# Kernel optimization log

Hardware: AMD Instinct MI355X
Metric: run time of the kernel (lower is better)

Reference implementation:

```python
import jax, jax.numpy as jnp
import numpy as np

N, E = 50000, 800000
IN_F, C, H, OUT_F = 128, 32, 4, 4
HC = H * C
EPS = 1e-5


def gatv2(x, src, dst, ea, Wl, Wr, We, att, bias, concat):
    # x: [N, in], ea: [E, 1], Wl/Wr: [in, H*C], We: [1, H*C], att: [h, C]
    h, c = att.shape
    xl = (x @ Wl).reshape(-1, h, c)          # [N, h, c]
    xr = (x @ Wr).reshape(-1, h, c)          # [N, h, c]
    m = xl[src] + xr[dst] + (ea @ We).reshape(-1, h, c)   # [E, h, c]
    e = jnp.einsum('ehc,hc->eh', jax.nn.leaky_relu(m, 0.2), att)  # [E, h]
    emax = jax.ops.segment_max(e, dst, num_segments=N)
    e = jnp.exp(e - emax[dst])
    denom = jax.ops.segment_sum(e, dst, num_segments=N)
    alpha = e / (denom[dst] + 1e-16)         # [E, h]
    out = jax.ops.segment_sum(alpha[:, :, None] * xl[src], dst, num_segments=N)  # [N, h, c]
    out = out.reshape(N, h * c) if concat else out.mean(axis=1)
    return out + bias


def bn_eval(x, g, b, m, v):
    return (x - m) * jax.lax.rsqrt(v + EPS) * g + b


def setup_inputs() -> dict:
    key = jax.random.key(0)
    ks = iter(jax.random.split(key, 40))
    nrm = lambda shape, s=0.2: jax.random.normal(next(ks), shape, jnp.float32) * s
    d = {}
    d['x'] = jax.random.normal(next(ks), (N, IN_F), jnp.float32)
    d['edge_index'] = jax.random.randint(next(ks), (2, E), 0, N, jnp.int32)
    d['edge_attr'] = jax.random.normal(next(ks), (E, 1), jnp.float32)
    # layer 1
    d['l1_Wl'] = nrm((IN_F, HC)); d['l1_Wr'] = nrm((IN_F, HC))
    d['l1_We'] = nrm((1, HC)); d['l1_att'] = nrm((H, C)); d['l1_b'] = nrm((HC,))
    # layers 2-9 stacked
    d['mid_Wl'] = nrm((8, HC, HC)); d['mid_Wr'] = nrm((8, HC, HC))
    d['mid_We'] = nrm((8, 1, HC)); d['mid_att'] = nrm((8, H, C)); d['mid_b'] = nrm((8, HC))
    # layer 10: heads=1, concat=False
    d['l10_Wl'] = nrm((HC, C)); d['l10_Wr'] = nrm((HC, C))
    d['l10_We'] = nrm((1, C)); d['l10_att'] = nrm((1, C)); d['l10_b'] = nrm((C,))
    # batchnorms (eval mode): bn1-9 stacked, bn10 separate
    d['bn_g'] = jax.random.uniform(next(ks), (9, HC), jnp.float32, 0.5, 1.5)
    d['bn_b'] = nrm((9, HC)); d['bn_m'] = nrm((9, HC))
    d['bn_v'] = jax.random.uniform(next(ks), (9, HC), jnp.float32, 0.5, 1.5)
    d['bn10_g'] = jax.random.uniform(next(ks), (C,), jnp.float32, 0.5, 1.5)
    d['bn10_b'] = nrm((C,)); d['bn10_m'] = nrm((C,))
    d['bn10_v'] = jax.random.uniform(next(ks), (C,), jnp.float32, 0.5, 1.5)
    d['lin_W'] = nrm((C, OUT_F)); d['lin_b'] = nrm((OUT_F,))
    return d


def reference(x, edge_index, edge_attr,
              l1_Wl, l1_Wr, l1_We, l1_att, l1_b,
              mid_Wl, mid_Wr, mid_We, mid_att, mid_b,
              l10_Wl, l10_Wr, l10_We, l10_att, l10_b,
              bn_g, bn_b, bn_m, bn_v,
              bn10_g, bn10_b, bn10_m, bn10_v,
              lin_W, lin_b):
    src, dst = edge_index[0], edge_index[1]
    h = jax.nn.relu(gatv2(x, src, dst, edge_attr, l1_Wl, l1_Wr, l1_We, l1_att, l1_b, True))
    h = bn_eval(h, bn_g[0], bn_b[0], bn_m[0], bn_v[0])
    for i in range(8):  # layers 2-9
        h = jax.nn.relu(gatv2(h, src, dst, edge_attr, mid_Wl[i], mid_Wr[i], mid_We[i], mid_att[i], mid_b[i], True))
        h = bn_eval(h, bn_g[i + 1], bn_b[i + 1], bn_m[i + 1], bn_v[i + 1])
    h = jax.nn.relu(gatv2(h, src, dst, edge_attr, l10_Wl, l10_Wr, l10_We, l10_att, l10_b, False))
    h = bn_eval(h, bn10_g, bn10_b, bn10_m, bn10_v)
    return h @ lin_W + lin_b
```

## Files before the change

### kernel.cpp

```cpp
#include <hip/hip_runtime.h>
#include <math.h>

#define NN 50000
#define EE 800000
#define EPS 1e-5f
#define SCAN_CH 196

#define NEG_BIG (-1e30f)
#define RESCALE_THR 4.0f

#define LO_SCALE 2048.0f
#define LO_INV   (1.0f/2048.0f)

typedef unsigned short u16;
typedef _Float16 f16x8 __attribute__((ext_vector_type(8)));
typedef float f32x4 __attribute__((ext_vector_type(4)));

__device__ __forceinline__ u16 f2h(float f) {
    _Float16 h = (_Float16)f;
    return __builtin_bit_cast(u16, h);
}
__device__ __forceinline__ float h2f(u16 u) {
    return (float)__builtin_bit_cast(_Float16, u);
}

__global__ void hist_kernel(const int* __restrict__ dst, int* cnt) {
    int e = blockIdx.x * blockDim.x + threadIdx.x;
    if (e < EE) atomicAdd(&cnt[dst[e]], 1);
}

__global__ void scan_part(const int* __restrict__ cnt, int* __restrict__ part) {
    __shared__ int red[256];
    int b = blockIdx.x, t = threadIdx.x;
    int i = b * SCAN_CH + t;
    int v = (t < SCAN_CH && i < NN) ? cnt[i] : 0;
    red[t] = v;
    __syncthreads();
#pragma unroll
    for (int s = 128; s; s >>= 1) {
        if (t < s) red[t] += red[t + s];
        __syncthreads();
    }
    if (t == 0) part[b] = red[0];
}

__global__ void scan_block(int* part) {
    __shared__ int buf[2][256];
    int t = threadIdx.x;
    int v = part[t];
    int p = 0;
    buf[0][t] = v;
    __syncthreads();
#pragma unroll
    for (int off = 1; off < 256; off <<= 1) {
        buf[p ^ 1][t] = buf[p][t] + ((t >= off) ? buf[p][t - off] : 0);
        __syncthreads();
        p ^= 1;
    }
    part[t] = buf[p][t] - v;
}

__global__ void scan_final(int* __restrict__ cntcur, const int* __restrict__ part,
                           int* __restrict__ row_start) {
    __shared__ int buf[2][256];
    int b = blockIdx.x, t = threadIdx.x;
    int i = b * SCAN_CH + t;
    int v = (t < SCAN_CH && i < NN) ? cntcur[i] : 0;
    int p = 0;
    buf[0][t] = v;
    __syncthreads();
#pragma unroll
    for (int off = 1; off < 256; off <<= 1) {
        buf[p ^ 1][t] = buf[p][t] + ((t >= off) ? buf[p][t - off] : 0);
        __syncthreads();
        p ^= 1;
    }
    if (t < SCAN_CH && i < NN) {
        int pos = part[b] + buf[p][t] - v;
        row_start[i] = pos;
        cntcur[i] = pos;
    }
    if (b == 0 && t == 0) row_start[NN] = EE;
}

__global__ void scatter_kernel(const int* __restrict__ ei, const float* __restrict__ ea,
                               int* cursor, int2* __restrict__ edge_pack) {
    int e = blockIdx.x * blockDim.x + threadIdx.x;
    if (e < EE) {
        int d = ei[EE + e];
        int pos = atomicAdd(&cursor[d], 1);
        edge_pack[pos] = make_int2(ei[e], __float_as_int(ea[e]));
    }
}

__global__ void split_f32(const float* __restrict__ in, u16* __restrict__ hi,
                          u16* __restrict__ lo, int n4) {
    int i = blockIdx.x * blockDim.x + threadIdx.x;
    if (i >= n4) return;
    float4 v = ((const float4*)in)[i];
    ushort4 h, l;
    h.x = f2h(v.x); l.x = f2h((v.x - h2f(h.x)) * LO_SCALE);
    h.y = f2h(v.y); l.y = f2h((v.y - h2f(h.y)) * LO_SCALE);
    h.z = f2h(v.z); l.z = f2h((v.z - h2f(h.z)) * LO_SCALE);
    h.w = f2h(v.w); l.w = f2h((v.w - h2f(h.w)) * LO_SCALE);
    ((ushort4*)hi)[i] = h;
    ((ushort4*)lo)[i] = l;
}

__global__ void conv_w(const float* __restrict__ l1Wl, const float* __restrict__ l1Wr,
                       const float* __restrict__ midWl, const float* __restrict__ midWr,
                       u16* __restrict__ Wh, u16* __restrict__ Wlo) {
    int tid = blockIdx.x * 256 + threadIdx.x;
    if (tid >= 9 * 256 * 128) return;
    int L = tid >> 15;
    int rem = tid & 32767;
    int n = rem >> 7, k = rem & 127;
    const float* WL;
    const float* WR;
    if (L == 0) { WL = l1Wl; WR = l1Wr; }
    else {
        WL = midWl + (size_t)(L - 1) * 16384;
        WR = midWr + (size_t)(L - 1) * 16384;
    }
    float w = (n < 128) ? WL[k * 128 + n] : WR[k * 128 + (n - 128)];
    u16 h = f2h(w);
    Wh[tid] = h;
    Wlo[tid] = f2h((w - h2f(h)) * LO_SCALE);
}

__global__ __launch_bounds__(256) void gemm_mfma(const u16* __restrict__ Ah,
                                                 const u16* __restrict__ Al,
                                                 const u16* __restrict__ Bh,
                                                 const u16* __restrict__ Bl,
                                                 float* __restrict__ C) {
    int w    = threadIdx.x >> 6;
    int lane = threadIdx.x & 63;
    int lr = lane & 15;
    int kg = lane >> 4;
    int rowbase = blockIdx.x * 128;
    int colbase = blockIdx.y * 128 + w * 32;

    f16x8 bh[2][4], bl[2][4];
#pragma unroll
    for (int ct = 0; ct < 2; ++ct) {
        size_t boff = (size_t)(colbase + ct * 16 + lr) * 128 + (size_t)(kg * 8);
#pragma unroll
        for (int ks = 0; ks < 4; ++ks) {
            bh[ct][ks] = *(const f16x8*)(Bh + boff + ks * 32);
            bl[ct][ks] = *(const f16x8*)(Bl + boff + ks * 32);
        }
    }

    auto aoff_of = [&](int rt) {
        int arow = rowbase + rt * 16 + lr;
        if (arow >= NN) arow = NN - 1;
        return (size_t)arow * 128 + (size_t)(kg * 8);
    };
    f16x8 ahc[4], alc[4], ahn[4], aln[4];
    {
        size_t ao = aoff_of(0);
#pragma unroll
        for (int ks = 0; ks < 4; ++ks) {
            ahc[ks] = *(const f16x8*)(Ah + ao + ks * 32);
            alc[ks] = *(const f16x8*)(Al + ao + ks * 32);
        }
    }

#pragma unroll
    for (int rt = 0; rt < 8; ++rt) {
        if (rt < 7) {
            size_t ao = aoff_of(rt + 1);
#pragma unroll
            for (int ks = 0; ks < 4; ++ks) {
                ahn[ks] = *(const f16x8*)(Ah + ao + ks * 32);
                aln[ks] = *(const f16x8*)(Al + ao + ks * 32);
            }
        }

        f32x4 aH[2], aL[2];
#pragma unroll
        for (int ct = 0; ct < 2; ++ct) {
            aH[ct] = (f32x4){0.f, 0.f, 0.f, 0.f};
            aL[ct] = (f32x4){0.f, 0.f, 0.f, 0.f};
        }
#pragma unroll
        for (int ks = 0; ks < 4; ++ks) {
#pragma unroll
            for (int ct = 0; ct < 2; ++ct) {
                aH[ct] = __builtin_amdgcn_mfma_f32_16x16x32_f16(ahc[ks], bh[ct][ks], aH[ct], 0, 0, 0);
                aL[ct] = __builtin_amdgcn_mfma_f32_16x16x32_f16(alc[ks], bh[ct][ks], aL[ct], 0, 0, 0);
                aL[ct] = __builtin_amdgcn_mfma_f32_16x16x32_f16(ahc[ks], bl[ct][ks], aL[ct], 0, 0, 0);
            }
        }

        int crow0 = rowbase + rt * 16 + kg * 4;
#pragma unroll
        for (int ct = 0; ct < 2; ++ct) {
            float* cp = C + (size_t)crow0 * 256 + colbase + ct * 16 + lr;
#pragma unroll
            for (int r = 0; r < 4; ++r) {
                if (crow0 + r < NN)
                    cp[(size_t)r * 256] = fmaf(aL[ct][r], LO_INV, aH[ct][r]);
            }
        }

        if (rt < 7) {
#pragma unroll
            for (int ks = 0; ks < 4; ++ks) { ahc[ks] = ahn[ks]; alc[ks] = aln[ks]; }
        }
    }
}

__global__ __launch_bounds__(256) void gemm_tile(const float* __restrict__ A,
                                                 const float* __restrict__ B,
                                                 float* __restrict__ C,
                                                 int M, int nc, int ldb, int ldc, int coff) {
    __shared__ float As[128][64];
    __shared__ float Bs[128][64];
    int t  = threadIdx.x;
    int bm = blockIdx.x * 64;
    int bn = blockIdx.y * 64;
    {
        int k4 = (t & 31) << 2;
        int r0 = t >> 5;
#pragma unroll
        for (int pass = 0; pass < 8; ++pass) {
            int row = r0 + pass * 8;
            int gm  = bm + row;
            float4 v = make_float4(0.f, 0.f, 0.f, 0.f);
            if (gm < M) v = *(const float4*)(A + (size_t)gm * 128 + k4);
            As[k4 + 0][row] = v.x; As[k4 + 1][row] = v.y;
            As[k4 + 2][row] = v.z; As[k4 + 3][row] = v.w;
        }
    }
    {
        int c4 = (t & 15) << 2;
        int kr = t >> 4;
#pragma unroll
        for (int pass = 0; pass < 8; ++pass) {
            int k  = kr + pass * 16;
            int gc = bn + c4;
            float4 v = make_float4(0.f, 0.f, 0.f, 0.f);
            if (gc < nc) v = *(const float4*)(B + (size_t)k * ldb + gc);
            *(float4*)&Bs[k][c4] = v;
        }
    }
    __syncthreads();

    int tx = t & 15, ty = t >> 4;
    int m0 = ty * 4, c0 = tx * 4;
    float acc[4][4] = {{0.f}};
#pragma unroll 8
    for (int k = 0; k < 128; ++k) {
        float4 av = *(const float4*)&As[k][m0];
        float4 bv = *(const float4*)&Bs[k][c0];
        float a4[4] = {av.x, av.y, av.z, av.w};
        float b4[4] = {bv.x, bv.y, bv.z, bv.w};
#pragma unroll
        for (int i = 0; i < 4; ++i)
#pragma unroll
            for (int j = 0; j < 4; ++j) acc[i][j] = fmaf(a4[i], b4[j], acc[i][j]);
    }
#pragma unroll
    for (int i = 0; i < 4; ++i) {
        int gm = bm + m0 + i;
        int gc = bn + c0;
        if (gm < M && gc < nc) {
            *(float4*)(C + (size_t)gm * ldc + coff + gc) =
                make_float4(acc[i][0], acc[i][1], acc[i][2], acc[i][3]);
        }
    }
}

__device__ __forceinline__ float dpp_add8(float x) {
    int t;
    t = __builtin_amdgcn_update_dpp(0, __float_as_int(x), 0xB1, 0xf, 0xf, true);
    x += __int_as_float(t);
    t = __builtin_amdgcn_update_dpp(0, __float_as_int(x), 0x4E, 0xf, 0xf, true);
    x += __int_as_float(t);
    t = __builtin_amdgcn_update_dpp(0, __float_as_int(x), 0x141, 0xf, 0xf, true);
    x += __int_as_float(t);
    return x;
}

__global__ __launch_bounds__(256) void node_agg_128(const float* __restrict__ xlr,
                                                    const int* __restrict__ row_start,
                                                    const int2* __restrict__ epack,
                                                    const float* __restrict__ We,
                                                    const float* __restrict__ att,
                                                    const float* __restrict__ bias,
                                                    const float* __restrict__ bng,
                                                    const float* __restrict__ bnb,
                                                    const float* __restrict__ bnm,
                                                    const float* __restrict__ bnv,
                                                    u16* __restrict__ ahi,
                                                    u16* __restrict__ alo,
                                                    int wf32,
                                                    float* __restrict__ hout) {
    int wave = (blockIdx.x * blockDim.x + threadIdx.x) >> 6;
    int lane = threadIdx.x & 63;
    if (wave >= NN) return;
    int half = lane >> 5;
    int c0   = (lane & 31) << 2;

    const float L2E = 1.44269504f;
    const float4 xr4 = *(const float4*)(xlr + (size_t)wave * 256 + 128 + c0);
    const float4 we4 = *(const float4*)(We + c0);
    const float4 at4 = *(const float4*)(att + c0);
    float4 a6, a4;
    a6.x = 0.6f * L2E * at4.x; a4.x = 0.4f * L2E * at4.x;
    a6.y = 0.6f * L2E * at4.y; a4.y = 0.4f * L2E * at4.y;
    a6.z = 0.6f * L2E * at4.z; a4.z = 0.4f * L2E * at4.z;
    a6.w = 0.6f * L2E * at4.w; a4.w = 0.4f * L2E * at4.w;

    int beg = row_start[wave], end = row_start[wave + 1];
    int lastE = end - 1;

    float mx0 = NEG_BIG, sm0 = 0.f;
    float mx1 = NEG_BIG, sm1 = 0.f;
    float4 ac0 = make_float4(0.f, 0.f, 0.f, 0.f);
    float4 ac1 = make_float4(0.f, 0.f, 0.f, 0.f);

    auto score = [&](float eav, const float4& xv) -> float {
        float m0 = xv.x + fmaf(eav, we4.x, xr4.x);
        float m1 = xv.y + fmaf(eav, we4.y, xr4.y);
        float m2 = xv.z + fmaf(eav, we4.z, xr4.z);
        float m3 = xv.w + fmaf(eav, we4.w, xr4.w);
        float p = fmaf(a6.x, m0, a4.x * fabsf(m0));
        p = fmaf(a6.y, m1, fmaf(a4.y, fabsf(m1), p));
        p = fmaf(a6.z, m2, fmaf(a4.z, fabsf(m2), p));
        p = fmaf(a6.w, m3, fmaf(a4.w, fabsf(m3), p));
        return dpp_add8(p);
    };

    auto upd = [&](float& mx, float& sm, float4& ac, float p, const float4& xv) {
        float d = p - mx;
        if (__ballot(d > RESCALE_THR)) {
            float nm = fmaxf(mx, p);
            float sc = exp2f(mx - nm);
            float w  = exp2f(p - nm);
            sm = fmaf(sm, sc, w);
            ac.x = fmaf(ac.x, sc, w * xv.x);
            ac.y = fmaf(ac.y, sc, w * xv.y);
            ac.z = fmaf(ac.z, sc, w * xv.z);
            ac.w = fmaf(ac.w, sc, w * xv.w);
            mx = nm;
        } else {
            float w = exp2f(d);
            sm += w;
            ac.x = fmaf(w, xv.x, ac.x);
            ac.y = fmaf(w, xv.y, ac.y);
            ac.z = fmaf(w, xv.z, ac.z);
            ac.w = fmaf(w, xv.w, ac.w);
        }
    };

    int j = beg;
    for (; j + 3 < end; j += 4) {
        int2 pkA = epack[j + half];
        int2 pkB = epack[j + 2 + half];
        float4 xA = *(const float4*)(xlr + ((size_t)pkA.x << 8) + c0);
        float4 xB = *(const float4*)(xlr + ((size_t)pkB.x << 8) + c0);
        float pA = score(__int_as_float(pkA.y), xA);
        float pB = score(__int_as_float(pkB.y), xB);
        upd(mx0, sm0, ac0, pA, xA);
        upd(mx1, sm1, ac1, pB, xB);
    }
    if (j < end) {
        int jeA = j + half;       bool dA = jeA > lastE; if (dA) jeA = lastE;
        int jeB = j + 2 + half;   bool dB = jeB > lastE; if (dB) jeB = lastE;
        int2 pkA = epack[jeA];
        int2 pkB = epack[jeB];
        float4 xA = *(const float4*)(xlr + ((size_t)pkA.x << 8) + c0);
        float4 xB = *(const float4*)(xlr + ((size_t)pkB.x << 8) + c0);
        float pA = score(__int_as_float(pkA.y), xA);
        float pB = score(__int_as_float(pkB.y), xB);
        pA = dA ? NEG_BIG : pA;
        pB = dB ? NEG_BIG : pB;
        upd(mx0, sm0, ac0, pA, xA);
        upd(mx1, sm1, ac1, pB, xB);
    }

    float Mx = fmaxf(mx0, mx1);
    float s0 = exp2f(mx0 - Mx), s1 = exp2f(mx1 - Mx);
    float sm = fmaf(sm0, s0, sm1 * s1);
    float4 ac;
    ac.x = fmaf(ac0.x, s0, ac1.x * s1);
    ac.y = fmaf(ac0.y, s0, ac1.y * s1);
    ac.z = fmaf(ac0.z, s0, ac1.z * s1);
    ac.w = fmaf(ac0.w, s0, ac1.w * s1);

    float  Mo  = __shfl_xor(Mx, 32);
    float  smo = __shfl_xor(sm, 32);
    float4 aco;
    aco.x = __shfl_xor(ac.x, 32);
    aco.y = __shfl_xor(ac.y, 32);
    aco.z = __shfl_xor(ac.z, 32);
    aco.w = __shfl_xor(ac.w, 32);
    float Mn = fmaxf(Mx, Mo);
    float ss = exp2f(Mx - Mn), so = exp2f(Mo - Mn);
    sm   = fmaf(sm, ss, smo * so);
    ac.x = fmaf(ac.x, ss, aco.x * so);
    ac.y = fmaf(ac.y, ss, aco.y * so);
    ac.z = fmaf(ac.z, ss, aco.z * so);
    ac.w = fmaf(ac.w, ss, aco.w * so);

    if (half == 0) {
        float inv = 1.f / (sm + 1e-16f);
        const float4 b4  = *(const float4*)(bias + c0);
        const float4 g4  = *(const float4*)(bng + c0);
        const float4 bb4 = *(const float4*)(bnb + c0);
        const float4 m4  = *(const float4*)(bnm + c0);
        const float4 v4  = *(const float4*)(bnv + c0);
        float4 y;
        y.x = fmaxf(fmaf(ac.x, inv, b4.x), 0.f);
        y.y = fmaxf(fmaf(ac.y, inv, b4.y), 0.f);
        y.z = fmaxf(fmaf(ac.z, inv, b4.z), 0.f);
        y.w = fmaxf(fmaf(ac.w, inv, b4.w), 0.f);
        y.x = (y.x - m4.x) * rsqrtf(v4.x + EPS) * g4.x + bb4.x;
        y.y = (y.y - m4.y) * rsqrtf(v4.y + EPS) * g4.y + bb4.y;
        y.z = (y.z - m4.z) * rsqrtf(v4.z + EPS) * g4.z + bb4.z;
        y.w = (y.w - m4.w) * rsqrtf(v4.w + EPS) * g4.w + bb4.w;

        ushort4 hh, ll;
        hh.x = f2h(y.x); ll.x = f2h((y.x - h2f(hh.x)) * LO_SCALE);
        hh.y = f2h(y.y); ll.y = f2h((y.y - h2f(hh.y)) * LO_SCALE);
        hh.z = f2h(y.z); ll.z = f2h((y.z - h2f(hh.z)) * LO_SCALE);
        hh.w = f2h(y.w); ll.w = f2h((y.w - h2f(hh.w)) * LO_SCALE);
        *(ushort4*)(ahi + (size_t)wave * 128 + c0) = hh;
        *(ushort4*)(alo + (size_t)wave * 128 + c0) = ll;
        if (wf32) *(float4*)(hout + (size_t)wave * 128 + c0) = y;
    }
}

__global__ __launch_bounds__(256) void node_agg_l10(const float* __restrict__ xlr,
                                                    const int* __restrict__ row_start,
                                                    const int2* __restrict__ epack,
                                                    const float* __restrict__ We,
                                                    const float* __restrict__ att,
                                                    const float* __restrict__ bias,
                                                    const float* __restrict__ bng,
                                                    const float* __restrict__ bnb,
                                                    const float* __restrict__ bnm,
                                                    const float* __restrict__ bnv,
                                                    const float* __restrict__ linW,
                                                    const float* __restrict__ linb,
                                                    float* __restrict__ out) {
    int n = (blockIdx.x * blockDim.x + threadIdx.x) >> 5;
    int c = threadIdx.x & 31;
    if (n >= NN) return;

    const float L2E = 1.44269504f;
    float xr = xlr[(size_t)n * 64 + 32 + c];
    float we = We[c];
    float a6 = 0.6f * L2E * att[c], a4 = 0.4f * L2E * att[c];
    int beg = row_start[n], end = row_start[n + 1];

    float mxs[2] = {-INFINITY, -INFINITY};
    float sms[2] = {0.f, 0.f};
    float acs[2] = {0.f, 0.f};

    auto upd = [&](int st, float xl, float eav) {
        float m = xl + fmaf(eav, we, xr);
        float p = fmaf(a6, m, a4 * fabsf(m));
#pragma unroll
        for (int off = 16; off; off >>= 1) p += __shfl_xor(p, off);
        float nm = fmaxf(mxs[st], p);
        float sc = exp2f(mxs[st] - nm);
        float w  = exp2f(p - nm);
        sms[st] = fmaf(sms[st], sc, w);
        acs[st] = fmaf(acs[st], sc, w * xl);
        mxs[st] = nm;
    };

    int j = beg;
    for (; j + 1 < end; j += 2) {
        int2 p0 = epack[j], p1 = epack[j + 1];
        float x0 = xlr[((size_t)p0.x << 6) + c];
        float x1 = xlr[((size_t)p1.x << 6) + c];
        upd(0, x0, __int_as_float(p0.y));
        upd(1, x1, __int_as_float(p1.y));
    }
    if (j < end) {
        int2 pk = epack[j];
        upd(0, xlr[((size_t)pk.x << 6) + c], __int_as_float(pk.y));
    }

    float M = fmaxf(mxs[0], mxs[1]);
    float sm = 0.f, acc = 0.f;
#pragma unroll
    for (int st = 0; st < 2; ++st) {
        float sc = (mxs[st] == -INFINITY) ? 0.f : exp2f(mxs[st] - M);
        sm  = fmaf(sms[st], sc, sm);
        acc = fmaf(acs[st], sc, acc);
    }

    float y = acc / (sm + 1e-16f) + bias[c];
    y = fmaxf(y, 0.f);
    y = (y - bnm[c]) * rsqrtf(bnv[c] + EPS) * bng[c] + bnb[c];

    float t0 = y * linW[c * 4 + 0];
    float t1 = y * linW[c * 4 + 1];
    float t2 = y * linW[c * 4 + 2];
    float t3 = y * linW[c * 4 + 3];
#pragma unroll
    for (int off = 16; off; off >>= 1) {
        t0 += __shfl_xor(t0, off);
        t1 += __shfl_xor(t1, off);
        t2 += __shfl_xor(t2, off);
        t3 += __shfl_xor(t3, off);
    }
    if (c == 0) {
        out[(size_t)n * 4 + 0] = t0 + linb[0];
        out[(size_t)n * 4 + 1] = t1 + linb[1];
        out[(size_t)n * 4 + 2] = t2 + linb[2];
        out[(size_t)n * 4 + 3] = t3 + linb[3];
    }
}

extern "C" void kernel_launch(void* const* d_in, const int* in_sizes, int n_in,
                              void* d_out, int out_size, void* d_ws, size_t ws_size,
                              hipStream_t stream) {
    const float* x      = (const float*)d_in[0];
    const int*   ei     = (const int*)d_in[1];
    const float* ea     = (const float*)d_in[2];
    const float* l1_Wl  = (const float*)d_in[3];
    const float* l1_Wr  = (const float*)d_in[4];
    const float* l1_We  = (const float*)d_in[5];
    const float* l1_att = (const float*)d_in[6];
    const float* l1_b   = (const float*)d_in[7];
    const float* mid_Wl = (const float*)d_in[8];
    const float* mid_Wr = (const float*)d_in[9];
    const float* mid_We = (const float*)d_in[10];
    const float* mid_att= (const float*)d_in[11];
    const float* mid_b  = (const float*)d_in[12];
    const float* l10_Wl = (const float*)d_in[13];
    const float* l10_Wr = (const float*)d_in[14];
    const float* l10_We = (const float*)d_in[15];
    const float* l10_att= (const float*)d_in[16];
    const float* l10_b  = (const float*)d_in[17];
    const float* bn_g   = (const float*)d_in[18];
    const float* bn_b   = (const float*)d_in[19];
    const float* bn_m   = (const float*)d_in[20];
    const float* bn_v   = (const float*)d_in[21];
    const float* bn10_g = (const float*)d_in[22];
    const float* bn10_b = (const float*)d_in[23];
    const float* bn10_m = (const float*)d_in[24];
    const float* bn10_v = (const float*)d_in[25];
    const float* lin_W  = (const float*)d_in[26];
    const float* lin_b  = (const float*)d_in[27];

    char* ws = (char*)d_ws;
    auto take = [&](size_t bytes) { char* p = ws; ws += (bytes + 255) & ~size_t(255); return p; };
    int*   row_start  = (int*)  take(sizeof(int) * (NN + 1));
    int*   cursor     = (int*)  take(sizeof(int) * NN);
    int*   part       = (int*)  take(sizeof(int) * 256);
    int2*  epack      = (int2*) take(sizeof(int2) * EE);
    float* xlr        = (float*)take(sizeof(float) * (size_t)NN * 256);
    float* h0         = (float*)take(sizeof(float) * (size_t)NN * 128);
    u16*   Ahi        = (u16*)  take(sizeof(u16) * (size_t)NN * 128);
    u16*   Alo        = (u16*)  take(sizeof(u16) * (size_t)NN * 128);
    u16*   Wthi       = (u16*)  take(sizeof(u16) * 9 * 256 * 128);
    u16*   Wtlo       = (u16*)  take(sizeof(u16) * 9 * 256 * 128);

    hipMemsetAsync(cursor, 0, sizeof(int) * NN, stream);
    hist_kernel<<<EE / 256, 256, 0, stream>>>(ei + EE, cursor);
    scan_part<<<256, 256, 0, stream>>>(cursor, part);
    scan_block<<<1, 256, 0, stream>>>(part);
    scan_final<<<256, 256, 0, stream>>>(cursor, part, row_start);
    scatter_kernel<<<EE / 256, 256, 0, stream>>>(ei, ea, cursor, epack);

    split_f32<<<(NN * 128 / 4 + 255) / 256, 256, 0, stream>>>(x, Ahi, Alo, NN * 128 / 4);
    conv_w<<<(9 * 256 * 128 + 255) / 256, 256, 0, stream>>>(l1_Wl, l1_Wr, mid_Wl, mid_Wr,
                                                            Wthi, Wtlo);

    const int GBM = (NN + 127) / 128;
    dim3 gmm(GBM, 2);

    gemm_mfma<<<gmm, 256, 0, stream>>>(Ahi, Alo, Wthi, Wtlo, xlr);
    node_agg_128<<<(NN * 64) / 256, 256, 0, stream>>>(
        xlr, row_start, epack, l1_We, l1_att, l1_b,
        bn_g, bn_b, bn_m, bn_v, Ahi, Alo, 0, h0);

    for (int i = 0; i < 8; ++i) {
        gemm_mfma<<<gmm, 256, 0, stream>>>(Ahi, Alo,
                                           Wthi + (size_t)(i + 1) * 32768,
                                           Wtlo + (size_t)(i + 1) * 32768, xlr);
        node_agg_128<<<(NN * 64) / 256, 256, 0, stream>>>(
            xlr, row_start, epack,
            mid_We + (size_t)i * 128, mid_att + (size_t)i * 128, mid_b + (size_t)i * 128,
            bn_g + (size_t)(i + 1) * 128, bn_b + (size_t)(i + 1) * 128,
            bn_m + (size_t)(i + 1) * 128, bn_v + (size_t)(i + 1) * 128,
            Ahi, Alo, (i == 7) ? 1 : 0, h0);
    }

    const int MB = (NN + 63) / 64;
    dim3 g1(MB, 1);
    gemm_tile<<<g1, 256, 0, stream>>>(h0, l10_Wl, xlr, NN, 32, 32, 64, 0);
    gemm_tile<<<g1, 256, 0, stream>>>(h0, l10_Wr, xlr, NN, 32, 32, 64, 32);
    node_agg_l10<<<(NN * 32 + 255) / 256, 256, 0, stream>>>(
        xlr, row_start, epack, l10_We, l10_att, l10_b,
        bn10_g, bn10_b, bn10_m, bn10_v, lin_W, lin_b, (float*)d_out);
}
```

Baseline: 1.249 ms.

## Split xl/xr into separate planes and process 4 edges per wave with prefetch

The GEMM output is now written as two separate N x 128 planes (xl and xr) instead of one interleaved 256-wide row, so gathered xl rows are contiguous 512-byte reads. The 128-channel aggregation kernel now handles 4 edges at a time per wave, with 16 lanes of 8 channels each, software prefetch of the next edge group, and a two-step cross-slot softmax merge. The final 32-channel layer gets the same 4-edge, float4-per-lane treatment with lazy rescaling and a DPP-based linear head. The aim is fewer loop iterations and more memory parallelism per node, at the cost of more registers per lane and more shuffle work at the end.

```diff
diff --git a/kernel.cpp b/kernel.cpp
--- a/kernel.cpp
+++ b/kernel.cpp
@@ -22,6 +22,25 @@
 }
 __device__ __forceinline__ float h2f(u16 u) {
     return (float)__builtin_bit_cast(_Float16, u);
+}
+
+__device__ __forceinline__ float dpp_add4(float x) {
+    int t;
+    t = __builtin_amdgcn_update_dpp(0, __float_as_int(x), 0xB1, 0xf, 0xf, true);
+    x += __int_as_float(t);
+    t = __builtin_amdgcn_update_dpp(0, __float_as_int(x), 0x4E, 0xf, 0xf, true);
+    x += __int_as_float(t);
+    return x;
+}
+__device__ __forceinline__ float dpp_add8(float x) {
+    int t;
+    t = __builtin_amdgcn_update_dpp(0, __float_as_int(x), 0xB1, 0xf, 0xf, true);
+    x += __int_as_float(t);
+    t = __builtin_amdgcn_update_dpp(0, __float_as_int(x), 0x4E, 0xf, 0xf, true);
+    x += __int_as_float(t);
+    t = __builtin_amdgcn_update_dpp(0, __float_as_int(x), 0x141, 0xf, 0xf, true);
+    x += __int_as_float(t);
+    return x;
 }
 
 __global__ void hist_kernel(const int* __restrict__ dst, int* cnt) {
@@ -138,7 +157,8 @@
     int lr = lane & 15;
     int kg = lane >> 4;
     int rowbase = blockIdx.x * 128;
-    int colbase = blockIdx.y * 128 + w * 32;
+    int colb = w * 32;
+    int colbase = blockIdx.y * 128 + colb;
 
     f16x8 bh[2][4], bl[2][4];
 #pragma unroll
@@ -166,6 +186,8 @@
         }
     }
 
+    float* Cp = C + (size_t)blockIdx.y * ((size_t)NN * 128);
+
 #pragma unroll
     for (int rt = 0; rt < 8; ++rt) {
         if (rt < 7) {
@@ -196,11 +218,11 @@
         int crow0 = rowbase + rt * 16 + kg * 4;
 #pragma unroll
         for (int ct = 0; ct < 2; ++ct) {
-            float* cp = C + (size_t)crow0 * 256 + colbase + ct * 16 + lr;
+            float* cp = Cp + (size_t)crow0 * 128 + colb + ct * 16 + lr;
 #pragma unroll
             for (int r = 0; r < 4; ++r) {
                 if (crow0 + r < NN)
-                    cp[(size_t)r * 256] = fmaf(aL[ct][r], LO_INV, aH[ct][r]);
+                    cp[(size_t)r * 128] = fmaf(aL[ct][r], LO_INV, aH[ct][r]);
             }
         }
 
@@ -270,17 +292,6 @@
                 make_float4(acc[i][0], acc[i][1], acc[i][2], acc[i][3]);
         }
     }
-}
-
-__device__ __forceinline__ float dpp_add8(float x) {
-    int t;
-    t = __builtin_amdgcn_update_dpp(0, __float_as_int(x), 0xB1, 0xf, 0xf, true);
-    x += __int_as_float(t);
-    t = __builtin_amdgcn_update_dpp(0, __float_as_int(x), 0x4E, 0xf, 0xf, true);
-    x += __int_as_float(t);
-    t = __builtin_amdgcn_update_dpp(0, __float_as_int(x), 0x141, 0xf, 0xf, true);
-    x += __int_as_float(t);
-    return x;
 }
 
 __global__ __launch_bounds__(256) void node_agg_128(const float* __restrict__ xlr,
@@ -300,136 +311,178 @@
     int wave = (blockIdx.x * blockDim.x + threadIdx.x) >> 6;
     int lane = threadIdx.x & 63;
     if (wave >= NN) return;
-    int half = lane >> 5;
-    int c0   = (lane & 31) << 2;
+    int slot = lane >> 4;
+    int c0   = (lane & 15) << 3;
+
+    const float* xlp = xlr;
+    const float* xrp = xlr + (size_t)NN * 128;
 
     const float L2E = 1.44269504f;
-    const float4 xr4 = *(const float4*)(xlr + (size_t)wave * 256 + 128 + c0);
-    const float4 we4 = *(const float4*)(We + c0);
-    const float4 at4 = *(const float4*)(att + c0);
-    float4 a6, a4;
-    a6.x = 0.6f * L2E * at4.x; a4.x = 0.4f * L2E * at4.x;
-    a6.y = 0.6f * L2E * at4.y; a4.y = 0.4f * L2E * at4.y;
-    a6.z = 0.6f * L2E * at4.z; a4.z = 0.4f * L2E * at4.z;
-    a6.w = 0.6f * L2E * at4.w; a4.w = 0.4f * L2E * at4.w;
+    const float4 xr0 = *(const float4*)(xrp + (size_t)wave * 128 + c0);
+    const float4 xr1 = *(const float4*)(xrp + (size_t)wave * 128 + c0 + 4);
+    const float4 we0 = *(const float4*)(We + c0);
+    const float4 we1 = *(const float4*)(We + c0 + 4);
+    const float4 at0 = *(const float4*)(att + c0);
+    const float4 at1 = *(const float4*)(att + c0 + 4);
+    float4 a60, a61, a40, a41;
+    a60.x = 0.6f * L2E * at0.x; a40.x = 0.4f * L2E * at0.x;
+    a60.y = 0.6f * L2E * at0.y; a40.y = 0.4f * L2E * at0.y;
+    a60.z = 0.6f * L2E * at0.z; a40.z = 0.4f * L2E * at0.z;
+    a60.w = 0.6f * L2E * at0.w; a40.w = 0.4f * L2E * at0.w;
+    a61.x = 0.6f * L2E * at1.x; a41.x = 0.4f * L2E * at1.x;
+    a61.y = 0.6f * L2E * at1.y; a41.y = 0.4f * L2E * at1.y;
+    a61.z = 0.6f * L2E * at1.z; a41.z = 0.4f * L2E * at1.z;
+    a61.w = 0.6f * L2E * at1.w; a41.w = 0.4f * L2E * at1.w;
 
     int beg = row_start[wave], end = row_start[wave + 1];
     int lastE = end - 1;
 
-    float mx0 = NEG_BIG, sm0 = 0.f;
-    float mx1 = NEG_BIG, sm1 = 0.f;
-    float4 ac0 = make_float4(0.f, 0.f, 0.f, 0.f);
-    float4 ac1 = make_float4(0.f, 0.f, 0.f, 0.f);
-
-    auto score = [&](float eav, const float4& xv) -> float {
-        float m0 = xv.x + fmaf(eav, we4.x, xr4.x);
-        float m1 = xv.y + fmaf(eav, we4.y, xr4.y);
-        float m2 = xv.z + fmaf(eav, we4.z, xr4.z);
-        float m3 = xv.w + fmaf(eav, we4.w, xr4.w);
-        float p = fmaf(a6.x, m0, a4.x * fabsf(m0));
-        p = fmaf(a6.y, m1, fmaf(a4.y, fabsf(m1), p));
-        p = fmaf(a6.z, m2, fmaf(a4.z, fabsf(m2), p));
-        p = fmaf(a6.w, m3, fmaf(a4.w, fabsf(m3), p));
-        return dpp_add8(p);
+    float mx = NEG_BIG, sm = 0.f;
+    float4 aA = make_float4(0.f, 0.f, 0.f, 0.f);
+    float4 aB = make_float4(0.f, 0.f, 0.f, 0.f);
+
+    auto score8 = [&](float eav, const float4& xa, const float4& xb) -> float {
+        float m0 = xa.x + fmaf(eav, we0.x, xr0.x);
+        float m1 = xa.y + fmaf(eav, we0.y, xr0.y);
+        float m2 = xa.z + fmaf(eav, we0.z, xr0.z);
+        float m3 = xa.w + fmaf(eav, we0.w, xr0.w);
+        float m4 = xb.x + fmaf(eav, we1.x, xr1.x);
+        float m5 = xb.y + fmaf(eav, we1.y, xr1.y);
+        float m6 = xb.z + fmaf(eav, we1.z, xr1.z);
+        float m7 = xb.w + fmaf(eav, we1.w, xr1.w);
+        float p = fmaf(a60.x, m0, a40.x * fabsf(m0));
+        p = fmaf(a60.y, m1, fmaf(a40.y, fabsf(m1), p));
+        p = fmaf(a60.z, m2, fmaf(a40.z, fabsf(m2), p));
+        p = fmaf(a60.w, m3, fmaf(a40.w, fabsf(m3), p));
+        p = fmaf(a61.x, m4, fmaf(a41.x, fabsf(m4), p));
+        p = fmaf(a61.y, m5, fmaf(a41.y, fabsf(m5), p));
+        p = fmaf(a61.z, m6, fmaf(a41.z, fabsf(m6), p));
+        p = fmaf(a61.w, m7, fmaf(a41.w, fabsf(m7), p));
+        return dpp_add4(p);
     };
 
-    auto upd = [&](float& mx, float& sm, float4& ac, float p, const float4& xv) {
+    auto upd = [&](float p, const float4& xa, const float4& xb) {
         float d = p - mx;
         if (__ballot(d > RESCALE_THR)) {
             float nm = fmaxf(mx, p);
             float sc = exp2f(mx - nm);
             float w  = exp2f(p - nm);
             sm = fmaf(sm, sc, w);
-            ac.x = fmaf(ac.x, sc, w * xv.x);
-            ac.y = fmaf(ac.y, sc, w * xv.y);
-            ac.z = fmaf(ac.z, sc, w * xv.z);
-            ac.w = fmaf(ac.w, sc, w * xv.w);
+            aA.x = fmaf(aA.x, sc, w * xa.x); aA.y = fmaf(aA.y, sc, w * xa.y);
+            aA.z = fmaf(aA.z, sc, w * xa.z); aA.w = fmaf(aA.w, sc, w * xa.w);
+            aB.x = fmaf(aB.x, sc, w * xb.x); aB.y = fmaf(aB.y, sc, w * xb.y);
+            aB.z = fmaf(aB.z, sc, w * xb.z); aB.w = fmaf(aB.w, sc, w * xb.w);
             mx = nm;
         } else {
             float w = exp2f(d);
             sm += w;
-            ac.x = fmaf(w, xv.x, ac.x);
-            ac.y = fmaf(w, xv.y, ac.y);
-            ac.z = fmaf(w, xv.z, ac.z);
-            ac.w = fmaf(w, xv.w, ac.w);
+            aA.x = fmaf(w, xa.x, aA.x); aA.y = fmaf(w, xa.y, aA.y);
+            aA.z = fmaf(w, xa.z, aA.z); aA.w = fmaf(w, xa.w, aA.w);
+            aB.x = fmaf(w, xb.x, aB.x); aB.y = fmaf(w, xb.y, aB.y);
+            aB.z = fmaf(w, xb.z, aB.z); aB.w = fmaf(w, xb.w, aB.w);
         }
     };
 
-    int j = beg;
-    for (; j + 3 < end; j += 4) {
-        int2 pkA = epack[j + half];
-        int2 pkB = epack[j + 2 + half];
-        float4 xA = *(const float4*)(xlr + ((size_t)pkA.x << 8) + c0);
-        float4 xB = *(const float4*)(xlr + ((size_t)pkB.x << 8) + c0);
-        float pA = score(__int_as_float(pkA.y), xA);
-        float pB = score(__int_as_float(pkB.y), xB);
-        upd(mx0, sm0, ac0, pA, xA);
-        upd(mx1, sm1, ac1, pB, xB);
-    }
-    if (j < end) {
-        int jeA = j + half;       bool dA = jeA > lastE; if (dA) jeA = lastE;
-        int jeB = j + 2 + half;   bool dB = jeB > lastE; if (dB) jeB = lastE;
-        int2 pkA = epack[jeA];
-        int2 pkB = epack[jeB];
-        float4 xA = *(const float4*)(xlr + ((size_t)pkA.x << 8) + c0);
-        float4 xB = *(const float4*)(xlr + ((size_t)pkB.x << 8) + c0);
-        float pA = score(__int_as_float(pkA.y), xA);
-        float pB = score(__int_as_float(pkB.y), xB);
-        pA = dA ? NEG_BIG : pA;
-        pB = dB ? NEG_BIG : pB;
-        upd(mx0, sm0, ac0, pA, xA);
-        upd(mx1, sm1, ac1, pB, xB);
-    }
-
-    float Mx = fmaxf(mx0, mx1);
-    float s0 = exp2f(mx0 - Mx), s1 = exp2f(mx1 - Mx);
-    float sm = fmaf(sm0, s0, sm1 * s1);
-    float4 ac;
-    ac.x = fmaf(ac0.x, s0, ac1.x * s1);
-    ac.y = fmaf(ac0.y, s0, ac1.y * s1);
-    ac.z = fmaf(ac0.z, s0, ac1.z * s1);
-    ac.w = fmaf(ac0.w, s0, ac1.w * s1);
-
-    float  Mo  = __shfl_xor(Mx, 32);
-    float  smo = __shfl_xor(sm, 32);
-    float4 aco;
-    aco.x = __shfl_xor(ac.x, 32);
-    aco.y = __shfl_xor(ac.y, 32);
-    aco.z = __shfl_xor(ac.z, 32);
-    aco.w = __shfl_xor(ac.w, 32);
-    float Mn = fmaxf(Mx, Mo);
-    float ss = exp2f(Mx - Mn), so = exp2f(Mo - Mn);
-    sm   = fmaf(sm, ss, smo * so);
-    ac.x = fmaf(ac.x, ss, aco.x * so);
-    ac.y = fmaf(ac.y, ss, aco.y * so);
-    ac.z = fmaf(ac.z, ss, aco.z * so);
-    ac.w = fmaf(ac.w, ss, aco.w * so);
-
-    if (half == 0) {
+    int nE = end - beg;
+    int last4 = beg + (nE & ~3);
+
+    int2 pkn; float4 xan, xbn;
+    if (beg < last4) {
+        pkn = epack[beg + slot];
+        const float* rp = xlp + ((size_t)pkn.x << 7) + c0;
+        xan = *(const float4*)rp;
+        xbn = *(const float4*)(rp + 4);
+    }
+    for (int j = beg; j < last4; ) {
+        int2 pk = pkn; float4 xa = xan, xb = xbn;
+        j += 4;
+        if (j < last4) {
+            pkn = epack[j + slot];
+            const float* rp = xlp + ((size_t)pkn.x << 7) + c0;
+            xan = *(const float4*)rp;
+            xbn = *(const float4*)(rp + 4);
+        }
+        float p = score8(__int_as_float(pk.y), xa, xb);
+        upd(p, xa, xb);
+    }
+    if (last4 < end) {
+        int je = last4 + slot;
+        bool dead = je > lastE; if (dead) je = lastE;
+        int2 pk = epack[je];
+        const float* rp = xlp + ((size_t)pk.x << 7) + c0;
+        float4 xa = *(const float4*)rp;
+        float4 xb = *(const float4*)(rp + 4);
+        float p = score8(__int_as_float(pk.y), xa, xb);
+        p = dead ? NEG_BIG : p;
+        upd(p, xa, xb);
+    }
+
+#pragma unroll
+    for (int off = 16; off <= 32; off <<= 1) {
+        float  Mo  = __shfl_xor(mx, off);
+        float  smo = __shfl_xor(sm, off);
+        float4 aAo, aBo;
+        aAo.x = __shfl_xor(aA.x, off); aAo.y = __shfl_xor(aA.y, off);
+        aAo.z = __shfl_xor(aA.z, off); aAo.w = __shfl_xor(aA.w, off);
+        aBo.x = __shfl_xor(aB.x, off); aBo.y = __shfl_xor(aB.y, off);
+        aBo.z = __shfl_xor(aB.z, off); aBo.w = __shfl_xor(aB.w, off);
+        float Mn = fmaxf(mx, Mo);
+        float ss = exp2f(mx - Mn), so = exp2f(Mo - Mn);
+        sm = fmaf(sm, ss, smo * so);
+        aA.x = fmaf(aA.x, ss, aAo.x * so); aA.y = fmaf(aA.y, ss, aAo.y * so);
+        aA.z = fmaf(aA.z, ss, aAo.z * so); aA.w = fmaf(aA.w, ss, aAo.w * so);
+        aB.x = fmaf(aB.x, ss, aBo.x * so); aB.y = fmaf(aB.y, ss, aBo.y * so);
+        aB.z = fmaf(aB.z, ss, aBo.z * so); aB.w = fmaf(aB.w, ss, aBo.w * so);
+        mx = Mn;
+    }
+
+    if (slot == 0) {
         float inv = 1.f / (sm + 1e-16f);
-        const float4 b4  = *(const float4*)(bias + c0);
-        const float4 g4  = *(const float4*)(bng + c0);
-        const float4 bb4 = *(const float4*)(bnb + c0);
-        const float4 m4  = *(const float4*)(bnm + c0);
-        const float4 v4  = *(const float4*)(bnv + c0);
-        float4 y;
-        y.x = fmaxf(fmaf(ac.x, inv, b4.x), 0.f);
-        y.y = fmaxf(fmaf(ac.y, inv, b4.y), 0.f);
-        y.z = fmaxf(fmaf(ac.z, inv, b4.z), 0.f);
-        y.w = fmaxf(fmaf(ac.w, inv, b4.w), 0.f);
-        y.x = (y.x - m4.x) * rsqrtf(v4.x + EPS) * g4.x + bb4.x;
-        y.y = (y.y - m4.y) * rsqrtf(v4.y + EPS) * g4.y + bb4.y;
-        y.z = (y.z - m4.z) * rsqrtf(v4.z + EPS) * g4.z + bb4.z;
-        y.w = (y.w - m4.w) * rsqrtf(v4.w + EPS) * g4.w + bb4.w;
-
-        ushort4 hh, ll;
-        hh.x = f2h(y.x); ll.x = f2h((y.x - h2f(hh.x)) * LO_SCALE);
-        hh.y = f2h(y.y); ll.y = f2h((y.y - h2f(hh.y)) * LO_SCALE);
-        hh.z = f2h(y.z); ll.z = f2h((y.z - h2f(hh.z)) * LO_SCALE);
-        hh.w = f2h(y.w); ll.w = f2h((y.w - h2f(hh.w)) * LO_SCALE);
-        *(ushort4*)(ahi + (size_t)wave * 128 + c0) = hh;
-        *(ushort4*)(alo + (size_t)wave * 128 + c0) = ll;
-        if (wf32) *(float4*)(hout + (size_t)wave * 128 + c0) = y;
+        const float4 b0 = *(const float4*)(bias + c0);
+        const float4 b1 = *(const float4*)(bias + c0 + 4);
+        const float4 g0 = *(const float4*)(bng + c0);
+        const float4 g1 = *(const float4*)(bng + c0 + 4);
+        const float4 q0 = *(const float4*)(bnb + c0);
+        const float4 q1 = *(const float4*)(bnb + c0 + 4);
+        const float4 m0 = *(const float4*)(bnm + c0);
+        const float4 m1 = *(const float4*)(bnm + c0 + 4);
+        const float4 v0 = *(const float4*)(bnv + c0);
+        const float4 v1 = *(const float4*)(bnv + c0 + 4);
+        float4 yA, yB;
+        yA.x = fmaxf(fmaf(aA.x, inv, b0.x), 0.f);
+        yA.y = fmaxf(fmaf(aA.y, inv, b0.y), 0.f);
+        yA.z = fmaxf(fmaf(aA.z, inv, b0.z), 0.f);
+        yA.w = fmaxf(fmaf(aA.w, inv, b0.w), 0.f);
+        yB.x = fmaxf(fmaf(aB.x, inv, b1.x), 0.f);
+        yB.y = fmaxf(fmaf(aB.y, inv, b1.y), 0.f);
+        yB.z = fmaxf(fmaf(aB.z, inv, b1.z), 0.f);
+        yB.w = fmaxf(fmaf(aB.w, inv, b1.w), 0.f);
+        yA.x = (yA.x - m0.x) * rsqrtf(v0.x + EPS) * g0.x + q0.x;
+        yA.y = (yA.y - m0.y) * rsqrtf(v0.y + EPS) * g0.y + q0.y;
+        yA.z = (yA.z - m0.z) * rsqrtf(v0.z + EPS) * g0.z + q0.z;
+        yA.w = (yA.w - m0.w) * rsqrtf(v0.w + EPS) * g0.w + q0.w;
+        yB.x = (yB.x - m1.x) * rsqrtf(v1.x + EPS) * g1.x + q1.x;
+        yB.y = (yB.y - m1.y) * rsqrtf(v1.y + EPS) * g1.y + q1.y;
+        yB.z = (yB.z - m1.z) * rsqrtf(v1.z + EPS) * g1.z + q1.z;
+        yB.w = (yB.w - m1.w) * rsqrtf(v1.w + EPS) * g1.w + q1.w;
+
+        ushort4 hA, lA, hB, lB;
+        hA.x = f2h(yA.x); lA.x = f2h((yA.x - h2f(hA.x)) * LO_SCALE);
+        hA.y = f2h(yA.y); lA.y = f2h((yA.y - h2f(hA.y)) * LO_SCALE);
+        hA.z = f2h(yA.z); lA.z = f2h((yA.z - h2f(hA.z)) * LO_SCALE);
+        hA.w = f2h(yA.w); lA.w = f2h((yA.w - h2f(hA.w)) * LO_SCALE);
+        hB.x = f2h(yB.x); lB.x = f2h((yB.x - h2f(hB.x)) * LO_SCALE);
+        hB.y = f2h(yB.y); lB.y = f2h((yB.y - h2f(hB.y)) * LO_SCALE);
+        hB.z = f2h(yB.z); lB.z = f2h((yB.z - h2f(hB.z)) * LO_SCALE);
+        hB.w = f2h(yB.w); lB.w = f2h((yB.w - h2f(hB.w)) * LO_SCALE);
+        *(ushort4*)(ahi + (size_t)wave * 128 + c0)     = hA;
+        *(ushort4*)(ahi + (size_t)wave * 128 + c0 + 4) = hB;
+        *(ushort4*)(alo + (size_t)wave * 128 + c0)     = lA;
+        *(ushort4*)(alo + (size_t)wave * 128 + c0 + 4) = lB;
+        if (wf32) {
+            *(float4*)(hout + (size_t)wave * 128 + c0)     = yA;
+            *(float4*)(hout + (size_t)wave * 128 + c0 + 4) = yB;
+        }
     }
 }
 
@@ -447,74 +500,133 @@
                                                     const float* __restrict__ linb,
                                                     float* __restrict__ out) {
     int n = (blockIdx.x * blockDim.x + threadIdx.x) >> 5;
-    int c = threadIdx.x & 31;
     if (n >= NN) return;
+    int q    = threadIdx.x & 31;
+    int slot = q >> 3;
+    int c0   = (q & 7) << 2;
 
     const float L2E = 1.44269504f;
-    float xr = xlr[(size_t)n * 64 + 32 + c];
-    float we = We[c];
-    float a6 = 0.6f * L2E * att[c], a4 = 0.4f * L2E * att[c];
+    const float4 xr = *(const float4*)(xlr + (size_t)n * 64 + 32 + c0);
+    const float4 we = *(const float4*)(We + c0);
+    const float4 at = *(const float4*)(att + c0);
+    float4 a6, a4;
+    a6.x = 0.6f * L2E * at.x; a4.x = 0.4f * L2E * at.x;
+    a6.y = 0.6f * L2E * at.y; a4.y = 0.4f * L2E * at.y;
+    a6.z = 0.6f * L2E * at.z; a4.z = 0.4f * L2E * at.z;
+    a6.w = 0.6f * L2E * at.w; a4.w = 0.4f * L2E * at.w;
+
     int beg = row_start[n], end = row_start[n + 1];
-
-    float mxs[2] = {-INFINITY, -INFINITY};
-    float sms[2] = {0.f, 0.f};
-    float acs[2] = {0.f, 0.f};
-
-    auto upd = [&](int st, float xl, float eav) {
-        float m = xl + fmaf(eav, we, xr);
-        float p = fmaf(a6, m, a4 * fabsf(m));
-#pragma unroll
-        for (int off = 16; off; off >>= 1) p += __shfl_xor(p, off);
-        float nm = fmaxf(mxs[st], p);
-        float sc = exp2f(mxs[st] - nm);
-        float w  = exp2f(p - nm);
-        sms[st] = fmaf(sms[st], sc, w);
-        acs[st] = fmaf(acs[st], sc, w * xl);
-        mxs[st] = nm;
+    int lastE = end - 1;
+
+    float mx = NEG_BIG, sm = 0.f;
+    float4 ac = make_float4(0.f, 0.f, 0.f, 0.f);
+
+    auto score4 = [&](float eav, const float4& xv) -> float {
+        float m0 = xv.x + fmaf(eav, we.x, xr.x);
+        float m1 = xv.y + fmaf(eav, we.y, xr.y);
+        float m2 = xv.z + fmaf(eav, we.z, xr.z);
+        float m3 = xv.w + fmaf(eav, we.w, xr.w);
+        float p = fmaf(a6.x, m0, a4.x * fabsf(m0));
+        p = fmaf(a6.y, m1, fmaf(a4.y, fabsf(m1), p));
+        p = fmaf(a6.z, m2, fmaf(a4.z, fabsf(m2), p));
+        p = fmaf(a6.w, m3, fmaf(a4.w, fabsf(m3), p));
+        return dpp_add8(p);
     };
 
-    int j = beg;
-    for (; j + 1 < end; j += 2) {
-        int2 p0 = epack[j], p1 = epack[j + 1];
-        float x0 = xlr[((size_t)p0.x << 6) + c];
-        float x1 = xlr[((size_t)p1.x << 6) + c];
-        upd(0, x0, __int_as_float(p0.y));
-        upd(1, x1, __int_as_float(p1.y));
-    }
-    if (j < end) {
-        int2 pk = epack[j];
-        upd(0, xlr[((size_t)pk.x << 6) + c], __int_as_float(pk.y));
-    }
-
-    float M = fmaxf(mxs[0], mxs[1]);
-    float sm = 0.f, acc = 0.f;
-#pragma unroll
-    for (int st = 0; st < 2; ++st) {
-        float sc = (mxs[st] == -INFINITY) ? 0.f : exp2f(mxs[st] - M);
-        sm  = fmaf(sms[st], sc, sm);
-        acc = fmaf(acs[st], sc, acc);
-    }
-
-    float y = acc / (sm + 1e-16f) + bias[c];
-    y = fmaxf(y, 0.f);
-    y = (y - bnm[c]) * rsqrtf(bnv[c] + EPS) * bng[c] + bnb[c];
-
-    float t0 = y * linW[c * 4 + 0];
-    float t1 = y * linW[c * 4 + 1];
-    float t2 = y * linW[c * 4 + 2];
-    float t3 = y * linW[c * 4 + 3];
-#pragma unroll
-    for (int off = 16; off; off >>= 1) {
-        t0 += __shfl_xor(t0, off);
-        t1 += __shfl_xor(t1, off);
-        t2 += __shfl_xor(t2, off);
-        t3 += __shfl_xor(t3, off);
-    }
-    if (c == 0) {
-        out[(size_t)n * 4 + 0] = t0 + linb[0];
-        out[(size_t)n * 4 + 1] = t1 + linb[1];
-        out[(size_t)n * 4 + 2] = t2 + linb[2];
-        out[(size_t)n * 4 + 3] = t3 + linb[3];
+    auto upd = [&](float p, const float4& xv) {
+        float d = p - mx;
+        if (__ballot(d > RESCALE_THR)) {
+            float nm = fmaxf(mx, p);
+            float sc = exp2f(mx - nm);
+            float w  = exp2f(p - nm);
+            sm = fmaf(sm, sc, w);
+            ac.x = fmaf(ac.x, sc, w * xv.x); ac.y = fmaf(ac.y, sc, w * xv.y);
+            ac.z = fmaf(ac.z, sc, w * xv.z); ac.w = fmaf(ac.w, sc, w * xv.w);
+            mx = nm;
+        } else {
+            float w = exp2f(d);
+            sm += w;
+            ac.x = fmaf(w, xv.x, ac.x); ac.y = fmaf(w, xv.y, ac.y);
+            ac.z = fmaf(w, xv.z, ac.z); ac.w = fmaf(w, xv.w, ac.w);
+        }
+    };
+
+    int nE = end - beg;
+    int last4 = beg + (nE & ~3);
+
+    int2 pkn; float4 xvn;
+    if (beg < last4) {
+        pkn = epack[beg + slot];
+        xvn = *(const float4*)(xlr + ((size_t)pkn.x << 6) + c0);
+    }
+    for (int j = beg; j < last4; ) {
+        int2 pk = pkn; float4 xv = xvn;
+        j += 4;
+        if (j < last4) {
+            pkn = epack[j + slot];
+            xvn = *(const float4*)(xlr + ((size_t)pkn.x << 6) + c0);
+        }
+        float p = score4(__int_as_float(pk.y), xv);
+        upd(p, xv);
+    }
+    if (last4 < end) {
+        int je = last4 + slot;
+        bool dead = je > lastE; if (dead) je = lastE;
+        int2 pk = epack[je];
+        float4 xv = *(const float4*)(xlr + ((size_t)pk.x << 6) + c0);
+        float p = score4(__int_as_float(pk.y), xv);
+        p = dead ? NEG_BIG : p;
+        upd(p, xv);
+    }
+
+#pragma unroll
+    for (int off = 8; off <= 16; off <<= 1) {
+        float  Mo  = __shfl_xor(mx, off);
+        float  smo = __shfl_xor(sm, off);
+        float4 aco;
+        aco.x = __shfl_xor(ac.x, off); aco.y = __shfl_xor(ac.y, off);
+        aco.z = __shfl_xor(ac.z, off); aco.w = __shfl_xor(ac.w, off);
+        float Mn = fmaxf(mx, Mo);
+        float ss = exp2f(mx - Mn), so = exp2f(Mo - Mn);
+        sm = fmaf(sm, ss, smo * so);
+        ac.x = fmaf(ac.x, ss, aco.x * so); ac.y = fmaf(ac.y, ss, aco.y * so);
+        ac.z = fmaf(ac.z, ss, aco.z * so); ac.w = fmaf(ac.w, ss, aco.w * so);
+        mx = Mn;
+    }
+
+    float inv = 1.f / (sm + 1e-16f);
+    const float4 b4 = *(const float4*)(bias + c0);
+    const float4 g4 = *(const float4*)(bng + c0);
+    const float4 q4 = *(const float4*)(bnb + c0);
+    const float4 m4 = *(const float4*)(bnm + c0);
+    const float4 v4 = *(const float4*)(bnv + c0);
+    float4 y;
+    y.x = fmaxf(fmaf(ac.x, inv, b4.x), 0.f);
+    y.y = fmaxf(fmaf(ac.y, inv, b4.y), 0.f);
+    y.z = fmaxf(fmaf(ac.z, inv, b4.z), 0.f);
+    y.w = fmaxf(fmaf(ac.w, inv, b4.w), 0.f);
+    y.x = (y.x - m4.x) * rsqrtf(v4.x + EPS) * g4.x + q4.x;
+    y.y = (y.y - m4.y) * rsqrtf(v4.y + EPS) * g4.y + q4.y;
+    y.z = (y.z - m4.z) * rsqrtf(v4.z + EPS) * g4.z + q4.z;
+    y.w = (y.w - m4.w) * rsqrtf(v4.w + EPS) * g4.w + q4.w;
+
+    const float4 w0 = *(const float4*)(linW + (c0 + 0) * 4);
+    const float4 w1 = *(const float4*)(linW + (c0 + 1) * 4);
+    const float4 w2 = *(const float4*)(linW + (c0 + 2) * 4);
+    const float4 w3 = *(const float4*)(linW + (c0 + 3) * 4);
+    float4 t;
+    t.x = fmaf(y.x, w0.x, fmaf(y.y, w1.x, fmaf(y.z, w2.x, y.w * w3.x)));
+    t.y = fmaf(y.x, w0.y, fmaf(y.y, w1.y, fmaf(y.z, w2.y, y.w * w3.y)));
+    t.z = fmaf(y.x, w0.z, fmaf(y.y, w1.z, fmaf(y.z, w2.z, y.w * w3.z)));
+    t.w = fmaf(y.x, w0.w, fmaf(y.y, w1.w, fmaf(y.z, w2.w, y.w * w3.w)));
+    t.x = dpp_add8(t.x); t.y = dpp_add8(t.y);
+    t.z = dpp_add8(t.z); t.w = dpp_add8(t.w);
+
+    if (q == 0) {
+        const float4 lb = *(const float4*)linb;
+        float4 o;
+        o.x = t.x + lb.x; o.y = t.y + lb.y; o.z = t.z + lb.z; o.w = t.w + lb.w;
+        *(float4*)(out + (size_t)n * 4) = o;
     }
 }
 
```

After: 1.327 ms. 1.06x slower.
